# Optimization experiments

Hardware: AMD Instinct MI355X
Metric: run time of the kernel (lower is better)

Reference implementation:

```python
import jax, jax.numpy as jnp
import numpy as np

B, S, D_MODEL, D_HEAD = 8, 2048, 1024, 128
MAX_ROUNDS = 3
THRESH = 0.1
SCALE = 1.0 / np.sqrt(float(D_HEAD))


def setup_inputs() -> dict:
    key = jax.random.key(0)
    ks = jax.random.split(key, 12)

    def lin(k, out_d, in_d):
        # torch Linear weight layout [out, in], y = x @ W.T + b
        return (jax.random.normal(k, (out_d, in_d), jnp.float32) / np.sqrt(float(in_d))).astype(jnp.float32)

    thesis_w = lin(ks[3], D_HEAD, D_HEAD)
    return {
        "x": jax.random.normal(ks[0], (B, S, D_MODEL), jnp.float32),
        "wq": lin(ks[1], D_HEAD, D_MODEL),
        "wk": lin(ks[2], D_HEAD, D_MODEL),
        "wv": lin(ks[4], D_HEAD, D_MODEL),
        "thesis_w": thesis_w,  # antithesis weight is -thesis_w per __init__
        "thesis_b": 0.02 * jax.random.normal(ks[5], (D_HEAD,), jnp.float32),
        "anti_b": 0.02 * jax.random.normal(ks[6], (D_HEAD,), jnp.float32),
        "s_w1": lin(ks[7], D_HEAD, 3 * D_HEAD),
        "s_b1": jnp.zeros((D_HEAD,), jnp.float32),
        "s_w2": lin(ks[8], D_HEAD, D_HEAD),
        "s_b2": jnp.zeros((D_HEAD,), jnp.float32),
        "g_w": lin(ks[9], 1, 2 * D_HEAD),
        "g_b": jnp.zeros((1,), jnp.float32),
    }


def reference(x, wq, wk, wv, thesis_w, thesis_b, anti_b, s_w1, s_b1, s_w2, s_b2, g_w, g_b):
    # q/k/v projections (no bias)
    q = jnp.einsum("bsm,hm->bsh", x, wq)
    k = jnp.einsum("bsm,hm->bsh", x, wk)
    v = jnp.einsum("bsm,hm->bsh", x, wv)

    attn = jax.nn.softmax(jnp.einsum("bqh,bkh->bqk", q, k) * SCALE, axis=-1)
    # dropout is identity at eval time
    cur = jnp.einsum("bqk,bkh->bqh", attn, v)  # [B,S,Dh]

    # attn_weights and v never change across rounds, so thesis/antithesis are
    # round-invariant: compute the context projections once.
    context = cur
    thesis = context @ thesis_w.T + thesis_b
    anti = context @ (-thesis_w).T + anti_b  # antithesis weight = -thesis weight

    active = jnp.ones((B, S), dtype=bool)
    for _ in range(MAX_ROUNDS):
        # emulate `if not active_mask.any(): break` under jit
        any_active = jnp.any(active)
        am = active[..., None].astype(x.dtype)
        at, aa, ac = thesis * am, anti * am, cur * am

        h = jax.nn.relu(jnp.concatenate([at, aa, ac], axis=-1) @ s_w1.T + s_b1)
        synth = h @ s_w2.T + s_b2
        gate = jax.nn.sigmoid(jnp.concatenate([ac, synth], axis=-1) @ g_w.T + g_b)
        update = gate * (synth - ac) * 0.1
        new = cur + update  # applied to ALL tokens, matching original

        stable = jnp.linalg.norm(update, axis=-1) < THRESH  # new - cur == update
        cur = jnp.where(any_active, new, cur)
        active = jnp.where(any_active, active & ~stable, active)
    return cur
```

## Files before the change

### kernel.cpp

```cpp
#include <hip/hip_runtime.h>
#include <hip/hip_bf16.h>

#define B_   8
#define S_   2048
#define DM   1024
#define DH   128
#define BS_  16384
#define SCALE_  0.08838834764831845f
#define SCALE2_ 0.12751744f

typedef unsigned short u16;
typedef unsigned int   u32;
typedef _Float16 half8 __attribute__((ext_vector_type(8)));
typedef __bf16   bf16x8 __attribute__((ext_vector_type(8)));
typedef float    f32x4 __attribute__((ext_vector_type(4)));
typedef u32      u32x4 __attribute__((ext_vector_type(4)));

union H8 { u32x4 v; u32 u[4]; half8 h; bf16x8 b; };

__device__ __forceinline__ float bf2f(u16 u) {
    union { u32 i; float f; } w; w.i = ((u32)u) << 16; return w.f;
}
__device__ __forceinline__ void unpack8(uint4 v, float* f) {
    f[0] = bf2f(v.x & 0xffff); f[1] = bf2f(v.x >> 16);
    f[2] = bf2f(v.y & 0xffff); f[3] = bf2f(v.y >> 16);
    f[4] = bf2f(v.z & 0xffff); f[5] = bf2f(v.z >> 16);
    f[6] = bf2f(v.w & 0xffff); f[7] = bf2f(v.w >> 16);
}
__device__ __forceinline__ float ldE(const void* b, size_t i, int isbf16) {
    return isbf16 ? bf2f(((const u16*)b)[i]) : ((const float*)b)[i];
}
__device__ __forceinline__ void ld8(const void* b, size_t i, int isbf16, float* f) {
    if (isbf16) {
        unpack8(*(const uint4*)((const u16*)b + i), f);
    } else {
        float4 a = *(const float4*)((const float*)b + i);
        float4 c = *(const float4*)((const float*)b + i + 4);
        f[0] = a.x; f[1] = a.y; f[2] = a.z; f[3] = a.w;
        f[4] = c.x; f[5] = c.y; f[6] = c.z; f[7] = c.w;
    }
}
__device__ __forceinline__ u32 f2pk(float v) {
    _Float16 h = (_Float16)v;
    _Float16 l = (_Float16)(v - (float)h);
    union { _Float16 f; u16 u; } a, b; a.f = h; b.f = l;
    return ((u32)a.u << 16) | (u32)b.u;
}
__device__ __forceinline__ void split8(const float* f, u32x4& hi, u32x4& lo) {
    u32 H[8], L[8];
#pragma unroll
    for (int j = 0; j < 8; ++j) {
        _Float16 h = (_Float16)f[j];
        _Float16 l = (_Float16)(f[j] - (float)h);
        union { _Float16 x; u16 u; } a, b; a.x = h; b.x = l;
        H[j] = a.u; L[j] = b.u;
    }
    hi = (u32x4){H[0] | (H[1] << 16), H[2] | (H[3] << 16), H[4] | (H[5] << 16), H[6] | (H[7] << 16)};
    lo = (u32x4){L[0] | (L[1] << 16), L[2] | (L[3] << 16), L[4] | (L[5] << 16), L[6] | (L[7] << 16)};
}
__device__ __forceinline__ u32 permHI(u32 eB, u32 eA) { return __builtin_amdgcn_perm(eB, eA, 0x07060302u); }
__device__ __forceinline__ u16 f2h(float v) { union { _Float16 f; u16 u; } a; a.f = (_Float16)v; return a.u; }
__device__ __forceinline__ float h2f(u16 u) { union { _Float16 f; u16 u; } a; a.u = u; return (float)a.f; }

__global__ void init_kernel(const void* x, int* flag, int* active, int* counts) {
    int i = blockIdx.x * 256 + threadIdx.x;
    if (i < BS_) active[i] = 1;
    if (i < 4) counts[i] = (i == 0) ? BS_ : 0;
    if (i == 0) {
        const u16* w = (const u16*)x;
        int sane = 0;
        for (int t = 0; t < 256; ++t) {
            int e = (w[2 * t] >> 7) & 0xFF;
            if (e >= 100 && e <= 135) ++sane;
        }
        *flag = (sane >= 192) ? 1 : 0;
    }
}

__global__ __launch_bounds__(256) void prepack_w_kernel(
    const void* __restrict__ wq, const void* __restrict__ wk, const void* __restrict__ wv,
    const int* __restrict__ flag, u32x4* __restrict__ wpk)
{
    const int isb = *flag;
    const int gid = blockIdx.x * 256 + threadIdx.x;
    const int l  = gid & 63;
    const int t  = (gid >> 6) & 7;
    const int ks = (gid >> 9) & 31;
    const int z  = gid >> 14;
    const void* W = (z == 0) ? wq : (z == 1) ? wk : wv;
    const int row = 16 * t + (l & 15);
    const int k0  = ks * 32 + 8 * (l >> 4);
    const size_t base = ((((size_t)z * 32 + ks) * 16) + 2 * t) * 64 + l;
    if (isb) {
        uint4 v = *(const uint4*)((const u16*)W + (size_t)row * DM + k0);
        wpk[base] = (u32x4){v.x, v.y, v.z, v.w};
    } else {
        float f[8];
        ld8(W, (size_t)row * DM + k0, 0, f);
        u32x4 hi, lo;
        split8(f, hi, lo);
        wpk[base]      = hi;
        wpk[base + 64] = lo;
    }
}

__global__ __launch_bounds__(256) void qkv_kernel(
    const void* __restrict__ x, const u32x4* __restrict__ wpk,
    const int* __restrict__ flag, u32* __restrict__ qout,
    u32x4* __restrict__ kfrag, u32x4* __restrict__ vfrag)
{
    const int isb = *flag;
    const int z = blockIdx.z;
    const int bx = blockIdx.x;
    const int m0 = ((bx & 7) * 32 + (bx >> 3)) * 64;
    const int tid = threadIdx.x;
    const int wave = tid >> 6, lane = tid & 63;
    const int qd = lane >> 4, c = lane & 15;

    __shared__ u32x4 WLraw[2][16][64];
    u32x4 (*WLb)[2][8][64] = (u32x4(*)[2][8][64])WLraw;
    u32x4 (*WLf)[8][2][64] = (u32x4(*)[8][2][64])WLraw;
    u16 (*TS)[136] = (u16(*)[136])WLraw;

    const u32x4* wz = wpk + (size_t)z * (32 * 16 * 64);
    const size_t arow = (size_t)(m0 + wave * 16 + c) * DM + 8 * qd;

#define STAGE2(i_, b_)                                                            \
    {                                                                             \
        _Pragma("unroll")                                                         \
        for (int _j = 0; _j < 4; ++_j) {                                          \
            const int _g = wave * 4 + _j, _ksub = _g >> 3, _t = _g & 7;           \
            __builtin_amdgcn_global_load_lds(                                     \
                (const __attribute__((address_space(1))) u32*)(                   \
                    wz + ((size_t)(2 * (i_) + _ksub) * 16 + 2 * _t) * 64 + lane), \
                (__attribute__((address_space(3))) u32*)&WLb[b_][_ksub][_t][0],   \
                16, 0, 0);                                                        \
        }                                                                         \
    }
#define STAGE_W(ks_, b_)                                                          \
    {                                                                             \
        const u32x4* _src = wz + ((size_t)(ks_) * 16 + 4 * wave) * 64 + lane;     \
        _Pragma("unroll")                                                         \
        for (int _j = 0; _j < 4; ++_j) {                                          \
            __builtin_amdgcn_global_load_lds(                                     \
                (const __attribute__((address_space(1))) u32*)(_src + _j * 64),   \
                (__attribute__((address_space(3))) u32*)&WLf[b_][2 * wave + (_j >> 1)][_j & 1][0], \
                16, 0, 0);                                                        \
        }                                                                         \
    }

    f32x4 acc[8] = {};

    if (isb) {
        const u16* xb = (const u16*)x;
        uint4 A0 = *(const uint4*)(xb + arow);
        uint4 A1 = *(const uint4*)(xb + arow + 32);
        STAGE2(0, 0);
        uint4 A0n = *(const uint4*)(xb + arow + 64);
        uint4 A1n = *(const uint4*)(xb + arow + 96);
        __syncthreads();
        for (int i = 0; i < 16; ++i) {
            const int cb = i & 1;
            if (i + 1 < 16) STAGE2(i + 1, cb ^ 1);
            H8 Ah0; Ah0.v = (u32x4){A0.x, A0.y, A0.z, A0.w};
            H8 Ah1; Ah1.v = (u32x4){A1.x, A1.y, A1.z, A1.w};
#pragma unroll
            for (int t = 0; t < 8; ++t) {
                H8 bh; bh.v = WLb[cb][0][t][lane];
                acc[t] = __builtin_amdgcn_mfma_f32_16x16x32_bf16(Ah0.b, bh.b, acc[t], 0, 0, 0);
            }
#pragma unroll
            for (int t = 0; t < 8; ++t) {
                H8 bh; bh.v = WLb[cb][1][t][lane];
                acc[t] = __builtin_amdgcn_mfma_f32_16x16x32_bf16(Ah1.b, bh.b, acc[t], 0, 0, 0);
            }
            A0 = A0n; A1 = A1n;
            if (i + 2 < 16) {
                A0n = *(const uint4*)(xb + arow + (size_t)(i + 2) * 64);
                A1n = *(const uint4*)(xb + arow + (size_t)(i + 2) * 64 + 32);
            }
            __syncthreads();
        }
    } else {
        float Ar[8], Arn[8];
        ld8(x, arow, 0, Ar);
        STAGE_W(0, 0);
        ld8(x, arow + 32, 0, Arn);
        __syncthreads();
        for (int ks = 0; ks < 32; ++ks) {
            const int cb = ks & 1;
            if (ks + 1 < 32) STAGE_W(ks + 1, cb ^ 1);
            H8 Ah, Al;
            split8(Ar, Ah.v, Al.v);
#pragma unroll
            for (int t = 0; t < 8; ++t) {
                H8 bh, bl;
                bh.v = WLf[cb][t][0][lane]; bl.v = WLf[cb][t][1][lane];
                acc[t] = __builtin_amdgcn_mfma_f32_16x16x32_f16(Al.h, bh.h, acc[t], 0, 0, 0);
                acc[t] = __builtin_amdgcn_mfma_f32_16x16x32_f16(Ah.h, bl.h, acc[t], 0, 0, 0);
                acc[t] = __builtin_amdgcn_mfma_f32_16x16x32_f16(Ah.h, bh.h, acc[t], 0, 0, 0);
            }
#pragma unroll
            for (int j = 0; j < 8; ++j) Ar[j] = Arn[j];
            if (ks + 2 < 32) ld8(x, arow + (size_t)(ks + 2) * 32, 0, Arn);
            __syncthreads();
        }
    }
#undef STAGE2
#undef STAGE_W

    if (z == 0) {
#pragma unroll
        for (int r = 0; r < 4; ++r) {
            const int row = m0 + wave * 16 + qd * 4 + r;
            u32* op = qout + (size_t)row * DH + c;
#pragma unroll
            for (int t = 0; t < 8; ++t) op[t * 16] = f2pk(acc[t][r]);
        }
    } else {
#pragma unroll
        for (int t = 0; t < 8; ++t)
#pragma unroll
            for (int r = 0; r < 4; ++r)
                TS[wave * 16 + qd * 4 + r][16 * t + c] = f2h(acc[t][r]);
        __syncthreads();
        if (z == 1) {
#pragma unroll
            for (int i = 0; i < 4; ++i) {
                const int f = tid + 256 * i;
                const int lf = f & 63, ks = (f >> 6) & 3, sub = f >> 8;
                const int key = sub * 16 + (lf & 15);
                const int d0  = ks * 32 + 8 * (lf >> 4);
                u32 w[4];
#pragma unroll
                for (int q = 0; q < 4; ++q)
                    w[q] = (u32)TS[key][d0 + 2 * q] | ((u32)TS[key][d0 + 2 * q + 1] << 16);
                kfrag[((size_t)(m0 / 16 + sub) * 4 + ks) * 64 + lf] = (u32x4){w[0], w[1], w[2], w[3]};
            }
        } else {
#pragma unroll
            for (int i = 0; i < 4; ++i) {
                const int f = tid + 256 * i;
                const int lf = f & 63, t = (f >> 6) & 7, sub = f >> 9;
                const int kb2 = sub * 32 + 8 * (lf >> 4);
                const int dh  = 16 * t + (lf & 15);
                u32 w[4];
#pragma unroll
                for (int q = 0; q < 4; ++q)
                    w[q] = (u32)TS[kb2 + 2 * q][dh] | ((u32)TS[kb2 + 2 * q + 1][dh] << 16);
                vfrag[((size_t)(m0 / 32 + sub) * 8 + t) * 64 + lf] = (u32x4){w[0], w[1], w[2], w[3]};
            }
        }
    }
}

template <bool WRITE_PARTIAL>
__device__ __forceinline__ void attn_body(
    const u32* qp, const u32x4* __restrict__ kfrag, const u32x4* __restrict__ vfrag,
    u16* outO, u16* outL, float* cur,
    int b, int q0, int kt0, int kt1, int part)
{
    const int tid = threadIdx.x;
    const int wave = tid >> 6, lane = tid & 63;
    const int qd = lane >> 4, c = lane & 15;

    __shared__ __align__(16) u16 PB[4][640];

    H8 Qh[4];
    {
        const u32* qr = qp + ((size_t)b * S_ + q0 + wave * 16 + c) * DH;
#pragma unroll
        for (int ks = 0; ks < 4; ++ks) {
            uint4 e0 = *(const uint4*)(qr + ks * 32 + qd * 8);
            uint4 e1 = *(const uint4*)(qr + ks * 32 + qd * 8 + 4);
            Qh[ks].u[0] = permHI(e0.y, e0.x); Qh[ks].u[1] = permHI(e0.w, e0.z);
            Qh[ks].u[2] = permHI(e1.y, e1.x); Qh[ks].u[3] = permHI(e1.w, e1.z);
        }
    }

    f32x4 O[8] = {};
    float lsum[4] = {};

    const u32x4* kb0 = kfrag + (size_t)b * 128 * 256;
    const u32x4* vb0 = vfrag + (size_t)b * 64 * 512;

    for (int kt = kt0; kt < kt1; ++kt) {
        const u32x4* kf = kb0 + (size_t)kt * 512;
        const u32x4* vf = vb0 + (size_t)kt * 512;

        f32x4 S0 = {}, S1 = {};
        __builtin_amdgcn_s_setprio(1);
#pragma unroll
        for (int ks = 0; ks < 4; ++ks) {
            H8 kh;
            kh.v = kf[ks * 64 + lane];
            S0 = __builtin_amdgcn_mfma_f32_16x16x32_f16(Qh[ks].h, kh.h, S0, 0, 0, 0);
            kh.v = kf[256 + ks * 64 + lane];
            S1 = __builtin_amdgcn_mfma_f32_16x16x32_f16(Qh[ks].h, kh.h, S1, 0, 0, 0);
        }
        __builtin_amdgcn_s_setprio(0);

        u16* pw = PB[wave];
#pragma unroll
        for (int r = 0; r < 4; ++r) {
            float e0 = exp2f(fmaf(S0[r], SCALE2_, -4.0f));
            float e1 = exp2f(fmaf(S1[r], SCALE2_, -4.0f));
            lsum[r] += e0 + e1;
            pw[(4 * qd + r) * 40 + c]      = f2h(e0);
            pw[(4 * qd + r) * 40 + 16 + c] = f2h(e1);
        }

        uint4 ev = *(const uint4*)&pw[c * 40 + 8 * qd];
        H8 Ph;
        Ph.u[0] = ev.x; Ph.u[1] = ev.y; Ph.u[2] = ev.z; Ph.u[3] = ev.w;

        __builtin_amdgcn_s_setprio(1);
#pragma unroll
        for (int t = 0; t < 8; ++t) {
            H8 vh;
            vh.v = vf[t * 64 + lane];
            O[t] = __builtin_amdgcn_mfma_f32_16x16x32_f16(Ph.h, vh.h, O[t], 0, 0, 0);
        }
        __builtin_amdgcn_s_setprio(0);
    }

    if (WRITE_PARTIAL) {
        float lred[4];
#pragma unroll
        for (int r = 0; r < 4; ++r) {
            float l = lsum[r];
            l += __shfl_xor(l, 1); l += __shfl_xor(l, 2);
            l += __shfl_xor(l, 4); l += __shfl_xor(l, 8);
            lred[r] = l;
        }
        const size_t rb = (size_t)b * S_ + q0 + wave * 16 + 4 * qd;
        u16* Op = outO + (size_t)part * ((size_t)BS_ * DH);
#pragma unroll
        for (int t = 0; t < 8; ++t)
#pragma unroll
            for (int r = 0; r < 4; ++r)
                Op[(rb + r) * DH + t * 16 + c] = f2h(O[t][r]);
        if (c == 0) {
            u16* lp = outL + (size_t)part * BS_;
#pragma unroll
            for (int r = 0; r < 4; ++r) lp[rb + r] = f2h(lred[r]);
        }
    } else {
        float linv[4];
#pragma unroll
        for (int r = 0; r < 4; ++r) {
            float l = lsum[r];
            l += __shfl_xor(l, 1); l += __shfl_xor(l, 2);
            l += __shfl_xor(l, 4); l += __shfl_xor(l, 8);
            linv[r] = 1.0f / l;
        }
        const size_t rb = (size_t)b * S_ + q0 + wave * 16 + 4 * qd;
#pragma unroll
        for (int t = 0; t < 8; ++t)
#pragma unroll
            for (int r = 0; r < 4; ++r)
                cur[(rb + r) * DH + t * 16 + c] = O[t][r] * linv[r];
    }
}

__global__ __launch_bounds__(256) void attn_kernel(
    const u32* qp, const u32x4* __restrict__ kfrag, const u32x4* __restrict__ vfrag, float* cur)
{
    const int rid = blockIdx.x + 32 * blockIdx.y;
    attn_body<false>(qp, kfrag, vfrag, nullptr, nullptr, cur,
                     rid & 7, ((rid >> 3) & 31) * 64, 0, S_ / 32, 0);
}

__global__ __launch_bounds__(256) void attn_split_kernel(
    const u32* qp, const u32x4* __restrict__ kfrag, const u32x4* __restrict__ vfrag,
    u16* __restrict__ Opart, u16* __restrict__ lpart)
{
    const int rid = blockIdx.x + 32 * (blockIdx.y + 8 * blockIdx.z);
    const int b    = rid & 7;
    const int qx   = (rid >> 3) & 31;
    const int part = rid >> 8;
    const int quart = S_ / 128;
    attn_body<true>(qp, kfrag, vfrag, Opart, lpart, nullptr,
                    b, qx * 64, part * quart, (part + 1) * quart, part);
}

__global__ __launch_bounds__(256) void prepack_rw_kernel(
    const void* __restrict__ tw, const void* __restrict__ w1, const void* __restrict__ w2,
    const int* __restrict__ flag, u32x4* __restrict__ pk)
{
    const int isb = *flag;
    const int gid = blockIdx.x * 256 + threadIdx.x;
    const int l = gid & 63, t = (gid >> 6) & 7, ks = (gid >> 9) & 3, mat = gid >> 11;
    const int row = 16 * t + (l & 15);
    const int k0  = ks * 32 + 8 * (l >> 4);
    float f[8];
    if (mat == 0)      ld8(tw, (size_t)row * DH + k0, isb, f);
    else if (mat <= 3) ld8(w1, (size_t)row * 384 + (mat - 1) * 128 + k0, isb, f);
    else               ld8(w2, (size_t)row * DH + k0, isb, f);
    u32x4 hi, lo;
    split8(f, hi, lo);
    const size_t base = (((size_t)mat * 4 + ks) * 16 + 2 * t) * 64 + l;
    pk[base] = hi; pk[base + 64] = lo;
}

struct Afrag { H8 h[4], l[4]; };
__device__ __forceinline__ void splitA(const float (&A)[4][8], Afrag& F) {
#pragma unroll
    for (int ks = 0; ks < 4; ++ks) split8(A[ks], F.h[ks].v, F.l[ks].v);
}

__global__ __launch_bounds__(256) void round0_kernel(
    const float* __restrict__ cur0g,
    const u16* __restrict__ Opart, const u16* __restrict__ lpart,
    const u32x4* __restrict__ pk, u16* __restrict__ T0,
    const void* __restrict__ tb, const void* __restrict__ ab,
    const void* __restrict__ b1, const void* __restrict__ b2,
    const void* __restrict__ gw, const void* __restrict__ gb,
    const int* __restrict__ flag, int* active, int* counts,
    float* cur_out, int combine)
{
    const int isb = *flag;
    const int tok0 = blockIdx.x * 16;
    const int tid = threadIdx.x;
    const int wave = tid >> 6, lane = tid & 63;
    const int qd = lane >> 4, c = lane & 15;

    __shared__ u32x4 WB[2][2][8][64];
    __shared__ u16 TS[16][132];
    __shared__ float CS[16][128];
    __shared__ float tbS[128], abS[128], b1S[128], b2S[128], gwS[256];
    __shared__ int blkcnt;

    auto stageBh = [&](int mat, int h) {
#pragma unroll
        for (int j = 0; j < 4; ++j) {
            const int g = wave * 4 + j, kl = g >> 3, t = g & 7;
            __builtin_amdgcn_global_load_lds(
                (const __attribute__((address_space(1))) u32*)(
                    pk + (((size_t)mat * 4 + 2 * h + kl) * 16 + 2 * t) * 64 + lane),
                (__attribute__((address_space(3))) u32*)&WB[h][kl][t][0],
                16, 0, 0);
        }
    };
    auto gemmBh = [&](const Afrag& F, int h, f32x4 (&acc)[2]) {
#pragma unroll
        for (int kl = 0; kl < 2; ++kl) {
            const int ks = 2 * h + kl;
#pragma unroll
            for (int tl = 0; tl < 2; ++tl) {
                H8 bh; bh.v = WB[h][kl][2 * wave + tl][lane];
                acc[tl] = __builtin_amdgcn_mfma_f32_16x16x32_f16(F.l[ks].h, bh.h, acc[tl], 0, 0, 0);
                acc[tl] = __builtin_amdgcn_mfma_f32_16x16x32_f16(F.h[ks].h, bh.h, acc[tl], 0, 0, 0);
            }
        }
    };
    auto stageFq = [&](int mat, int q, int buf) {
#pragma unroll
        for (int j = 0; j < 4; ++j) {
            const int g = wave * 4 + j, p = g & 1, t = g >> 1;
            __builtin_amdgcn_global_load_lds(
                (const __attribute__((address_space(1))) u32*)(
                    pk + (((size_t)mat * 4 + q) * 16 + 2 * t + p) * 64 + lane),
                (__attribute__((address_space(3))) u32*)&WB[buf][p][t][0],
                16, 0, 0);
        }
    };
    auto gemmFq = [&](const Afrag& F, int q, int buf, f32x4 (&acc)[2]) {
#pragma unroll
        for (int tl = 0; tl < 2; ++tl) {
            H8 bh, bl;
            bh.v = WB[buf][0][2 * wave + tl][lane];
            bl.v = WB[buf][1][2 * wave + tl][lane];
            acc[tl] = __builtin_amdgcn_mfma_f32_16x16x32_f16(F.l[q].h, bh.h, acc[tl], 0, 0, 0);
            acc[tl] = __builtin_amdgcn_mfma_f32_16x16x32_f16(F.h[q].h, bl.h, acc[tl], 0, 0, 0);
            acc[tl] = __builtin_amdgcn_mfma_f32_16x16x32_f16(F.h[q].h, bh.h, acc[tl], 0, 0, 0);
        }
    };
    auto GEMMF = [&](int mat, const Afrag& F, f32x4 (&acc)[2]) {
        for (int q = 0; q < 4; ++q) {
            stageFq(mat, q, q & 1);
            __syncthreads();
            gemmFq(F, q, q & 1, acc);
            __syncthreads();
        }
    };

    const int hr = 4 * qd;
    const int rowl = c;

    auto writeTS = [&](const f32x4 (&acc)[2], const float* bias, bool relu) {
#pragma unroll
        for (int tl = 0; tl < 2; ++tl)
#pragma unroll
            for (int rr = 0; rr < 4; ++rr) {
                const int col = 16 * (2 * wave + tl) + c;
                float v = acc[tl][rr] + (bias ? bias[col] : 0.0f);
                TS[hr + rr][col] = f2h(relu ? fmaxf(v, 0.0f) : v);
            }
    };
    auto buildA1 = [&](Afrag& F) {
        float Ac[4][8];
#pragma unroll
        for (int ks = 0; ks < 4; ++ks)
#pragma unroll
            for (int j = 0; j < 8; ++j)
                Ac[ks][j] = CS[rowl][ks * 32 + 8 * qd + j];
        splitA(Ac, F);
    };
    auto buildAt = [&](Afrag& F) {
        float Ac[4][8];
#pragma unroll
        for (int ks = 0; ks < 4; ++ks)
#pragma unroll
            for (int j = 0; j < 8; ++j) {
                const int k = ks * 32 + 8 * qd + j;
                Ac[ks][j] = h2f(TS[rowl][k]) + tbS[k];
            }
        splitA(Ac, F);
    };
    auto buildAa = [&](Afrag& F) {
        float Ac[4][8];
#pragma unroll
        for (int ks = 0; ks < 4; ++ks)
#pragma unroll
            for (int j = 0; j < 8; ++j) {
                const int k = ks * 32 + 8 * qd + j;
                Ac[ks][j] = abS[k] - h2f(TS[rowl][k]);
            }
        splitA(Ac, F);
    };
    auto buildAh = [&](Afrag& F) {
        float Ac[4][8];
#pragma unroll
        for (int ks = 0; ks < 4; ++ks)
#pragma unroll
            for (int j = 0; j < 8; ++j)
                Ac[ks][j] = h2f(TS[rowl][ks * 32 + 8 * qd + j]);
        splitA(Ac, F);
    };

    if (tid < 128) {
        tbS[tid] = ldE(tb, tid, isb); abS[tid] = ldE(ab, tid, isb);
        b1S[tid] = ldE(b1, tid, isb); b2S[tid] = ldE(b2, tid, isb);
    }
    gwS[tid] = ldE(gw, tid, isb);
    if (tid == 0) blkcnt = 0;
    const float gbf = ldE(gb, 0, isb);
    {
        const int row = tid >> 4, d0 = (tid & 15) * 8;
        float a8[8];
        if (combine) {
            const size_t grow = (size_t)(tok0 + row);
            const float lt = h2f(lpart[grow]) + h2f(lpart[BS_ + grow])
                           + h2f(lpart[2 * BS_ + grow]) + h2f(lpart[3 * BS_ + grow]);
            const float linv = 1.0f / lt;
            float acc[8] = {};
            const size_t N1 = (size_t)BS_ * DH;
#pragma unroll
            for (int p = 0; p < 4; ++p) {
                const u16* op = Opart + (size_t)p * N1 + grow * DH + d0;
                uint4 v0 = *(const uint4*)op;
                const u32 w[4] = {v0.x, v0.y, v0.z, v0.w};
#pragma unroll
                for (int j = 0; j < 4; ++j) {
                    acc[2 * j]     += h2f((u16)(w[j] & 0xffff));
                    acc[2 * j + 1] += h2f((u16)(w[j] >> 16));
                }
            }
#pragma unroll
            for (int e = 0; e < 8; ++e) a8[e] = acc[e] * linv;
        } else {
            const float* cr = cur0g + (size_t)(tok0 + row) * DH + d0;
            float4 v0 = *(const float4*)cr;
            float4 v1 = *(const float4*)(cr + 4);
            a8[0] = v0.x; a8[1] = v0.y; a8[2] = v0.z; a8[3] = v0.w;
            a8[4] = v1.x; a8[5] = v1.y; a8[6] = v1.z; a8[7] = v1.w;
        }
#pragma unroll
        for (int e = 0; e < 8; ++e) CS[row][d0 + e] = a8[e];
    }

    if (isb) {
        stageBh(0, 0);
        __syncthreads();
        Afrag FA; buildA1(FA);
        stageBh(0, 1);
        f32x4 accT[2] = {};
        gemmBh(FA, 0, accT);
        __syncthreads();
        stageBh(1, 0);
        gemmBh(FA, 1, accT);
        writeTS(accT, nullptr, false);
        __syncthreads();
        for (int i = tid; i < 16 * 64; i += 256) {
            const int row = i >> 6, c2 = (i & 63) * 2;
            *(u32*)&T0[(size_t)(tok0 + row) * DH + c2] = *(const u32*)&TS[row][c2];
        }
        f32x4 acc1[2] = {};
        {
            Afrag FC; buildAt(FC);
            stageBh(1, 1);
            gemmBh(FC, 0, acc1);
            __syncthreads();
            stageBh(2, 0);
            gemmBh(FC, 1, acc1);
            __syncthreads();
        }
        {
            Afrag FC; buildAa(FC);
            stageBh(2, 1);
            gemmBh(FC, 0, acc1);
            __syncthreads();
            stageBh(3, 0);
            gemmBh(FC, 1, acc1);
            __syncthreads();
        }
        {
            Afrag FC; buildA1(FC);
            stageBh(3, 1);
            gemmBh(FC, 0, acc1);
            __syncthreads();
            stageBh(4, 0);
            gemmBh(FC, 1, acc1);
        }
        writeTS(acc1, b1S, true);
        __syncthreads();
        {
            Afrag FC; buildAh(FC);
            stageBh(4, 1);
            f32x4 acc2[2] = {};
            gemmBh(FC, 0, acc2);
            __syncthreads();
            gemmBh(FC, 1, acc2);
            writeTS(acc2, b2S, false);
        }
        __syncthreads();
    } else {
        __syncthreads();
        Afrag FA; buildA1(FA);
        f32x4 accT[2] = {};
        GEMMF(0, FA, accT);
        writeTS(accT, nullptr, false);
        __syncthreads();
        for (int i = tid; i < 16 * 64; i += 256) {
            const int row = i >> 6, c2 = (i & 63) * 2;
            *(u32*)&T0[(size_t)(tok0 + row) * DH + c2] = *(const u32*)&TS[row][c2];
        }
        f32x4 acc1[2] = {};
        { Afrag FC; buildAt(FC); GEMMF(1, FC, acc1); }
        { Afrag FC; buildAa(FC); GEMMF(2, FC, acc1); }
        { Afrag FC; buildA1(FC); GEMMF(3, FC, acc1); }
        writeTS(acc1, b1S, true);
        __syncthreads();
        {
            Afrag FC; buildAh(FC);
            f32x4 acc2[2] = {};
            GEMMF(4, FC, acc2);
            writeTS(acc2, b2S, false);
        }
        __syncthreads();
    }

    const int tok = tid >> 4, d0g = (tid & 15) * 8;
    float cv[8];
#pragma unroll
    for (int e = 0; e < 8; ++e) cv[e] = CS[tok][d0g + e];
    float srow[8];
#pragma unroll
    for (int e = 0; e < 8; ++e) srow[e] = h2f(TS[tok][d0g + e]);
    float gp = 0.0f;
#pragma unroll
    for (int e = 0; e < 8; ++e)
        gp += cv[e] * gwS[d0g + e] + srow[e] * gwS[128 + d0g + e];
    gp += __shfl_xor(gp, 1, 16);
    gp += __shfl_xor(gp, 2, 16);
    gp += __shfl_xor(gp, 4, 16);
    gp += __shfl_xor(gp, 8, 16);
    const float gate = 1.0f / (1.0f + __expf(-(gp + gbf)));
    float ss = 0.0f; float up[8];
#pragma unroll
    for (int e = 0; e < 8; ++e) {
        float u = gate * (srow[e] - cv[e]) * 0.1f;
        up[e] = u; ss += u * u;
    }
    ss += __shfl_xor(ss, 1, 16);
    ss += __shfl_xor(ss, 2, 16);
    ss += __shfl_xor(ss, 4, 16);
    ss += __shfl_xor(ss, 8, 16);
    const bool stable = sqrtf(ss) < 0.1f;

    float* op = cur_out + (size_t)(tok0 + tok) * DH + d0g;
    *(float4*)op       = make_float4(cv[0] + up[0], cv[1] + up[1], cv[2] + up[2], cv[3] + up[3]);
    *(float4*)(op + 4) = make_float4(cv[4] + up[4], cv[5] + up[5], cv[6] + up[6], cv[7] + up[7]);
    const int newact = stable ? 0 : 1;
    if ((tid & 15) == 0) {
        active[tok0 + tok] = newact;
        if (newact) atomicAdd(&blkcnt, 1);
    }
    __syncthreads();
    if (tid == 0 && blkcnt > 0) atomicAdd(&counts[1], blkcnt);
}

__global__ __launch_bounds__(256) void round_kernel(
    const float* curr,
    const u32x4* __restrict__ pk, const u16* __restrict__ T0,
    const void* __restrict__ tb, const void* __restrict__ ab,
    const void* __restrict__ b1, const void* __restrict__ b2,
    const void* __restrict__ gw, const void* __restrict__ gb,
    const int* __restrict__ flag, int* active, int* counts, int r,
    float* cur_out, void* dout)
{
    const int isb = *flag;
    const int tok0 = blockIdx.x * 32;
    const int tid = threadIdx.x;
    const bool last = (dout != nullptr);

    if (counts[r] <= 0) {
        if (last) {
            for (int e = tid; e < 32 * DH; e += 256) {
                size_t idx = (size_t)tok0 * DH + e;
                float v = curr[idx];
                if (isb) ((__hip_bfloat16*)dout)[idx] = __float2bfloat16(v);
                else     ((float*)dout)[idx] = v;
            }
        }
        return;
    }

    const int wave = tid >> 6, lane = tid & 63;
    const int qd = lane >> 4, c = lane & 15;
    const int rowg = wave >> 1, colh = wave & 1;

    __shared__ u32x4 WB[2][4][8][64];
    __shared__ u16 TS[32][132];
    __shared__ float actS[32], tbS[128], abS[128], b1S[128], b2S[128], gwS[256];
    __shared__ int blkcnt;

    auto stageB = [&](int mat, int buf) {
#pragma unroll
        for (int j = 0; j < 8; ++j) {
            const int g = wave * 8 + j, ks = g >> 3, t = g & 7;
            __builtin_amdgcn_global_load_lds(
                (const __attribute__((address_space(1))) u32*)(
                    pk + (((size_t)mat * 4 + ks) * 16 + 2 * t) * 64 + lane),
                (__attribute__((address_space(3))) u32*)&WB[buf][ks][t][0],
                16, 0, 0);
        }
    };
    auto stageF = [&](int mat, int h, int buf) {
#pragma unroll
        for (int j = 0; j < 8; ++j) {
            const int g = wave * 8 + j, kl = g >> 4, p = (g >> 3) & 1, t = g & 7;
            __builtin_amdgcn_global_load_lds(
                (const __attribute__((address_space(1))) u32*)(
                    pk + (((size_t)mat * 4 + 2 * h + kl) * 16 + 2 * t + p) * 64 + lane),
                (__attribute__((address_space(3))) u32*)&WB[buf][kl * 2 + p][t][0],
                16, 0, 0);
        }
    };
    auto gemmB = [&](const Afrag& F, int buf, f32x4 (&acc)[4]) {
#pragma unroll
        for (int ks = 0; ks < 4; ++ks)
#pragma unroll
            for (int tl = 0; tl < 4; ++tl) {
                H8 bh; bh.v = WB[buf][ks][4 * colh + tl][lane];
                acc[tl] = __builtin_amdgcn_mfma_f32_16x16x32_f16(F.l[ks].h, bh.h, acc[tl], 0, 0, 0);
                acc[tl] = __builtin_amdgcn_mfma_f32_16x16x32_f16(F.h[ks].h, bh.h, acc[tl], 0, 0, 0);
            }
    };
    auto gemmFh = [&](const Afrag& F, int h, int buf, f32x4 (&acc)[4]) {
#pragma unroll
        for (int kl = 0; kl < 2; ++kl) {
            const int ks = 2 * h + kl;
#pragma unroll
            for (int tl = 0; tl < 4; ++tl) {
                H8 bh, bl;
                bh.v = WB[buf][kl * 2][4 * colh + tl][lane];
                bl.v = WB[buf][kl * 2 + 1][4 * colh + tl][lane];
                acc[tl] = __builtin_amdgcn_mfma_f32_16x16x32_f16(F.l[ks].h, bh.h, acc[tl], 0, 0, 0);
                acc[tl] = __builtin_amdgcn_mfma_f32_16x16x32_f16(F.h[ks].h, bl.h, acc[tl], 0, 0, 0);
                acc[tl] = __builtin_amdgcn_mfma_f32_16x16x32_f16(F.h[ks].h, bh.h, acc[tl], 0, 0, 0);
            }
        }
    };
    auto STAGE = [&](int mat, int buf) { if (isb) stageB(mat, buf); else stageF(mat, 0, buf); };
    auto GEMM = [&](int mat, const Afrag& F, int buf, f32x4 (&acc)[4]) {
        if (isb) {
            gemmB(F, buf, acc);
        } else {
            gemmFh(F, 0, buf, acc);
            __syncthreads();
            stageF(mat, 1, buf);
            __syncthreads();
            gemmFh(F, 1, buf, acc);
        }
    };

    STAGE(1, 1);
    if (tid < 32) actS[tid] = active[tok0 + tid] ? 1.0f : 0.0f;
    if (tid < 128) {
        tbS[tid] = ldE(tb, tid, isb); abS[tid] = ldE(ab, tid, isb);
        b1S[tid] = ldE(b1, tid, isb); b2S[tid] = ldE(b2, tid, isb);
    }
    gwS[tid] = ldE(gw, tid, isb);
    if (tid == 0) blkcnt = 0;
    const float gbf = ldE(gb, 0, isb);

    const int rowl = 16 * rowg + c;
    const int hr   = 16 * rowg + 4 * qd;

    for (int i = tid; i < 32 * 64; i += 256) {
        const int row = i >> 6, c2 = (i & 63) * 2;
        *(u32*)&TS[row][c2] = *(const u32*)&T0[(size_t)(tok0 + row) * DH + c2];
    }
    __syncthreads();

    STAGE(2, 0);
    f32x4 acc1[4] = {};
    const float am_r = actS[rowl];
    {
        float Ac[4][8];
#pragma unroll
        for (int ks = 0; ks < 4; ++ks)
#pragma unroll
            for (int j = 0; j < 8; ++j) {
                const int k = ks * 32 + 8 * qd + j;
                Ac[ks][j] = (h2f(TS[rowl][k]) + tbS[k]) * am_r;
            }
        Afrag FC; splitA(Ac, FC);
        GEMM(1, FC, 1, acc1);
    }
    __syncthreads();

    STAGE(3, 1);
    {
        float Ac[4][8];
#pragma unroll
        for (int ks = 0; ks < 4; ++ks)
#pragma unroll
            for (int j = 0; j < 8; ++j) {
                const int k = ks * 32 + 8 * qd + j;
                Ac[ks][j] = (abS[k] - h2f(TS[rowl][k])) * am_r;
            }
        Afrag FC; splitA(Ac, FC);
        GEMM(2, FC, 0, acc1);
    }
    __syncthreads();

    STAGE(4, 0);
    {
        float Ac[4][8];
        const float* cr = curr + (size_t)(tok0 + rowl) * DH;
#pragma unroll
        for (int ks = 0; ks < 4; ++ks) {
            float4 a0 = *(const float4*)(cr + ks * 32 + 8 * qd);
            float4 a1 = *(const float4*)(cr + ks * 32 + 8 * qd + 4);
            Ac[ks][0] = a0.x * am_r; Ac[ks][1] = a0.y * am_r;
            Ac[ks][2] = a0.z * am_r; Ac[ks][3] = a0.w * am_r;
            Ac[ks][4] = a1.x * am_r; Ac[ks][5] = a1.y * am_r;
            Ac[ks][6] = a1.z * am_r; Ac[ks][7] = a1.w * am_r;
        }
        Afrag FC; splitA(Ac, FC);
        GEMM(3, FC, 1, acc1);
    }
#pragma unroll
    for (int tl = 0; tl < 4; ++tl)
#pragma unroll
        for (int rr = 0; rr < 4; ++rr) {
            const int col = 16 * (4 * colh + tl) + c;
            TS[hr + rr][col] = f2h(fmaxf(acc1[tl][rr] + b1S[col], 0.0f));
        }
    __syncthreads();

    {
        float Ac[4][8];
#pragma unroll
        for (int ks = 0; ks < 4; ++ks)
#pragma unroll
            for (int j = 0; j < 8; ++j)
                Ac[ks][j] = h2f(TS[rowl][ks * 32 + 8 * qd + j]);
        Afrag FC; splitA(Ac, FC);
        f32x4 acc2[4] = {};
        GEMM(4, FC, 0, acc2);
        __syncthreads();
#pragma unroll
        for (int tl = 0; tl < 4; ++tl)
#pragma unroll
            for (int rr = 0; rr < 4; ++rr) {
                const int col = 16 * (4 * colh + tl) + c;
                TS[hr + rr][col] = f2h(acc2[tl][rr] + b2S[col]);
            }
    }
    __syncthreads();

    const int tok = tid >> 3, d0 = (tid & 7) * 16;
    const float am = actS[tok];
    const float* cp = curr + (size_t)(tok0 + tok) * DH + d0;
    float cv[16];
#pragma unroll
    for (int t = 0; t < 4; ++t) {
        float4 vv = *(const float4*)(cp + t * 4);
        cv[t * 4] = vv.x; cv[t * 4 + 1] = vv.y; cv[t * 4 + 2] = vv.z; cv[t * 4 + 3] = vv.w;
    }
    float srow[16];
#pragma unroll
    for (int e = 0; e < 16; ++e) srow[e] = h2f(TS[tok][d0 + e]);
    float gp = 0.0f;
#pragma unroll
    for (int e = 0; e < 16; ++e)
        gp += cv[e] * am * gwS[d0 + e] + srow[e] * gwS[128 + d0 + e];
    gp += __shfl_xor(gp, 1, 8);
    gp += __shfl_xor(gp, 2, 8);
    gp += __shfl_xor(gp, 4, 8);
    const float gate = 1.0f / (1.0f + __expf(-(gp + gbf)));
    float ss = 0.0f; float up[16];
#pragma unroll
    for (int e = 0; e < 16; ++e) {
        float u = gate * (srow[e] - cv[e] * am) * 0.1f;
        up[e] = u; ss += u * u;
    }
    ss += __shfl_xor(ss, 1, 8);
    ss += __shfl_xor(ss, 2, 8);
    ss += __shfl_xor(ss, 4, 8);
    const bool stable = sqrtf(ss) < 0.1f;

    if (last) {
        size_t off = (size_t)(tok0 + tok) * DH + d0;
        if (isb) {
            __hip_bfloat16* op = (__hip_bfloat16*)dout + off;
#pragma unroll
            for (int e = 0; e < 16; ++e) op[e] = __float2bfloat16(cv[e] + up[e]);
        } else {
            float* op = (float*)dout + off;
#pragma unroll
            for (int t = 0; t < 4; ++t)
                *(float4*)(op + t * 4) = make_float4(cv[t * 4] + up[t * 4], cv[t * 4 + 1] + up[t * 4 + 1],
                                                     cv[t * 4 + 2] + up[t * 4 + 2], cv[t * 4 + 3] + up[t * 4 + 3]);
        }
    } else {
        float* op = cur_out + (size_t)(tok0 + tok) * DH + d0;
#pragma unroll
        for (int t = 0; t < 4; ++t)
            *(float4*)(op + t * 4) = make_float4(cv[t * 4] + up[t * 4], cv[t * 4 + 1] + up[t * 4 + 1],
                                                 cv[t * 4 + 2] + up[t * 4 + 2], cv[t * 4 + 3] + up[t * 4 + 3]);
    }
    const int newact = (am > 0.0f && !stable) ? 1 : 0;
    if ((tid & 7) == 0) {
        active[tok0 + tok] = newact;
        if (newact) atomicAdd(&blkcnt, 1);
    }
    __syncthreads();
    if (tid == 0 && blkcnt > 0) atomicAdd(&counts[r + 1], blkcnt);
}

extern "C" void kernel_launch(void* const* d_in, const int* in_sizes, int n_in,
                              void* d_out, int out_size, void* d_ws, size_t ws_size,
                              hipStream_t stream) {
    const void* x  = d_in[0];
    const void* wq = d_in[1];
    const void* wk = d_in[2];
    const void* wv = d_in[3];
    const void* tw = d_in[4];
    const void* tb = d_in[5];
    const void* ab = d_in[6];
    const void* w1 = d_in[7];
    const void* b1 = d_in[8];
    const void* w2 = d_in[9];
    const void* b2 = d_in[10];
    const void* gw = d_in[11];
    const void* gb = d_in[12];

    u32* ws = (u32*)d_ws;
    const size_t N1 = (size_t)BS_ * DH;
    u32* qp = ws;
    u32* kp = ws + N1;
    u32* vp = ws + 2 * N1;
    int* active = (int*)(ws + 3 * N1);
    int* counts = active + BS_;
    int* flag   = counts + 4;
    float* cur0  = (float*)qp;
    float* cur_r = (float*)kp;
    u16* Opart16 = (u16*)(ws + 3 * N1 + 32768);
    u16* lpart16 = (u16*)(ws + 5 * N1 + 32768);
    const bool big_ws = ws_size >= (size_t)42300000;
    u32x4* wpk = (u32x4*)(ws + 3 * N1 + 32768);
    u32x4* pkRW = (u32x4*)vp;
    u16*   T0c  = (u16*)(vp + 131072);
    u32x4* kfragP = (u32x4*)kp;
    u32x4* vfragP = (u32x4*)vp;

    init_kernel<<<dim3(BS_ / 256), 256, 0, stream>>>(x, flag, active, counts);
    prepack_w_kernel<<<dim3(192), 256, 0, stream>>>(wq, wk, wv, flag, wpk);
    qkv_kernel<<<dim3(BS_ / 64, 1, 3), 256, 0, stream>>>(x, wpk, flag, qp, kfragP, vfragP);
    if (big_ws) {
        attn_split_kernel<<<dim3(S_ / 64, B_, 4), 256, 0, stream>>>(qp, kfragP, vfragP, Opart16, lpart16);
    } else {
        attn_kernel<<<dim3(S_ / 64, B_), 256, 0, stream>>>(qp, kfragP, vfragP, cur0);
    }
    prepack_rw_kernel<<<dim3(40), 256, 0, stream>>>(tw, w1, w2, flag, pkRW);
    round0_kernel<<<dim3(BS_ / 16), 256, 0, stream>>>(
        cur0, Opart16, lpart16, pkRW, T0c, tb, ab, b1, b2, gw, gb,
        flag, active, counts, cur_r, big_ws ? 1 : 0);
    round_kernel<<<dim3(BS_ / 32), 256, 0, stream>>>(
        cur_r, pkRW, T0c, tb, ab, b1, b2, gw, gb, flag, active, counts, 1, cur_r, nullptr);
    round_kernel<<<dim3(BS_ / 32), 256, 0, stream>>>(
        cur_r, pkRW, T0c, tb, ab, b1, b2, gw, gb, flag, active, counts, 2, cur_r, d_out);
}
```

Measured before the change: 253.2 us.

## Split QKV projection tile across 8 waves, halving per-wave output columns

The QKV projection kernel now launches 512 threads per block instead of 256. Pairs of waves share a 16-row group, and each wave computes half of the 128 output columns, holding 4 accumulators instead of 8. Weight staging into LDS and the fragment writeback loops are redistributed over the larger thread count. The aim is more waves in flight to hide latency and fewer accumulator registers per wave. The cost is that each A row fragment is now loaded from global memory by two waves, and 512-thread blocks may limit how many blocks fit per CU.

```diff
diff --git a/kernel.cpp b/kernel.cpp
--- a/kernel.cpp
+++ b/kernel.cpp
@@ -104,7 +104,7 @@
     }
 }
 
-__global__ __launch_bounds__(256) void qkv_kernel(
+__global__ __launch_bounds__(512) void qkv_kernel(
     const void* __restrict__ x, const u32x4* __restrict__ wpk,
     const int* __restrict__ flag, u32* __restrict__ qout,
     u32x4* __restrict__ kfrag, u32x4* __restrict__ vfrag)
@@ -116,6 +116,7 @@
     const int tid = threadIdx.x;
     const int wave = tid >> 6, lane = tid & 63;
     const int qd = lane >> 4, c = lane & 15;
+    const int rowg = wave >> 1, colh = wave & 1;
 
     __shared__ u32x4 WLraw[2][16][64];
     u32x4 (*WLb)[2][8][64] = (u32x4(*)[2][8][64])WLraw;
@@ -123,13 +124,13 @@
     u16 (*TS)[136] = (u16(*)[136])WLraw;
 
     const u32x4* wz = wpk + (size_t)z * (32 * 16 * 64);
-    const size_t arow = (size_t)(m0 + wave * 16 + c) * DM + 8 * qd;
+    const size_t arow = (size_t)(m0 + 16 * rowg + c) * DM + 8 * qd;
 
 #define STAGE2(i_, b_)                                                            \
     {                                                                             \
         _Pragma("unroll")                                                         \
-        for (int _j = 0; _j < 4; ++_j) {                                          \
-            const int _g = wave * 4 + _j, _ksub = _g >> 3, _t = _g & 7;           \
+        for (int _j = 0; _j < 2; ++_j) {                                          \
+            const int _g = wave * 2 + _j, _ksub = _g >> 3, _t = _g & 7;           \
             __builtin_amdgcn_global_load_lds(                                     \
                 (const __attribute__((address_space(1))) u32*)(                   \
                     wz + ((size_t)(2 * (i_) + _ksub) * 16 + 2 * _t) * 64 + lane), \
@@ -139,17 +140,18 @@
     }
 #define STAGE_W(ks_, b_)                                                          \
     {                                                                             \
-        const u32x4* _src = wz + ((size_t)(ks_) * 16 + 4 * wave) * 64 + lane;     \
         _Pragma("unroll")                                                         \
-        for (int _j = 0; _j < 4; ++_j) {                                          \
+        for (int _j = 0; _j < 2; ++_j) {                                          \
+            const int _s = wave * 2 + _j;                                         \
             __builtin_amdgcn_global_load_lds(                                     \
-                (const __attribute__((address_space(1))) u32*)(_src + _j * 64),   \
-                (__attribute__((address_space(3))) u32*)&WLf[b_][2 * wave + (_j >> 1)][_j & 1][0], \
+                (const __attribute__((address_space(1))) u32*)(                   \
+                    wz + ((size_t)(ks_) * 16 + _s) * 64 + lane),                  \
+                (__attribute__((address_space(3))) u32*)&WLf[b_][_s >> 1][_s & 1][0], \
                 16, 0, 0);                                                        \
         }                                                                         \
     }
 
-    f32x4 acc[8] = {};
+    f32x4 acc[4] = {};
 
     if (isb) {
         const u16* xb = (const u16*)x;
@@ -165,14 +167,14 @@
             H8 Ah0; Ah0.v = (u32x4){A0.x, A0.y, A0.z, A0.w};
             H8 Ah1; Ah1.v = (u32x4){A1.x, A1.y, A1.z, A1.w};
 #pragma unroll
-            for (int t = 0; t < 8; ++t) {
-                H8 bh; bh.v = WLb[cb][0][t][lane];
-                acc[t] = __builtin_amdgcn_mfma_f32_16x16x32_bf16(Ah0.b, bh.b, acc[t], 0, 0, 0);
-            }
-#pragma unroll
-            for (int t = 0; t < 8; ++t) {
-                H8 bh; bh.v = WLb[cb][1][t][lane];
-                acc[t] = __builtin_amdgcn_mfma_f32_16x16x32_bf16(Ah1.b, bh.b, acc[t], 0, 0, 0);
+            for (int tl = 0; tl < 4; ++tl) {
+                H8 bh; bh.v = WLb[cb][0][4 * colh + tl][lane];
+                acc[tl] = __builtin_amdgcn_mfma_f32_16x16x32_bf16(Ah0.b, bh.b, acc[tl], 0, 0, 0);
+            }
+#pragma unroll
+            for (int tl = 0; tl < 4; ++tl) {
+                H8 bh; bh.v = WLb[cb][1][4 * colh + tl][lane];
+                acc[tl] = __builtin_amdgcn_mfma_f32_16x16x32_bf16(Ah1.b, bh.b, acc[tl], 0, 0, 0);
             }
             A0 = A0n; A1 = A1n;
             if (i + 2 < 16) {
@@ -193,12 +195,13 @@
             H8 Ah, Al;
             split8(Ar, Ah.v, Al.v);
 #pragma unroll
-            for (int t = 0; t < 8; ++t) {
+            for (int tl = 0; tl < 4; ++tl) {
                 H8 bh, bl;
-                bh.v = WLf[cb][t][0][lane]; bl.v = WLf[cb][t][1][lane];
-                acc[t] = __builtin_amdgcn_mfma_f32_16x16x32_f16(Al.h, bh.h, acc[t], 0, 0, 0);
-                acc[t] = __builtin_amdgcn_mfma_f32_16x16x32_f16(Ah.h, bl.h, acc[t], 0, 0, 0);
-                acc[t] = __builtin_amdgcn_mfma_f32_16x16x32_f16(Ah.h, bh.h, acc[t], 0, 0, 0);
+                bh.v = WLf[cb][4 * colh + tl][0][lane];
+                bl.v = WLf[cb][4 * colh + tl][1][lane];
+                acc[tl] = __builtin_amdgcn_mfma_f32_16x16x32_f16(Al.h, bh.h, acc[tl], 0, 0, 0);
+                acc[tl] = __builtin_amdgcn_mfma_f32_16x16x32_f16(Ah.h, bl.h, acc[tl], 0, 0, 0);
+                acc[tl] = __builtin_amdgcn_mfma_f32_16x16x32_f16(Ah.h, bh.h, acc[tl], 0, 0, 0);
             }
 #pragma unroll
             for (int j = 0; j < 8; ++j) Ar[j] = Arn[j];
@@ -212,22 +215,22 @@
     if (z == 0) {
 #pragma unroll
         for (int r = 0; r < 4; ++r) {
-            const int row = m0 + wave * 16 + qd * 4 + r;
-            u32* op = qout + (size_t)row * DH + c;
-#pragma unroll
-            for (int t = 0; t < 8; ++t) op[t * 16] = f2pk(acc[t][r]);
+            const int row = m0 + 16 * rowg + 4 * qd + r;
+            u32* op = qout + (size_t)row * DH + 64 * colh + c;
+#pragma unroll
+            for (int tl = 0; tl < 4; ++tl) op[tl * 16] = f2pk(acc[tl][r]);
         }
     } else {
 #pragma unroll
-        for (int t = 0; t < 8; ++t)
+        for (int tl = 0; tl < 4; ++tl)
 #pragma unroll
             for (int r = 0; r < 4; ++r)
-                TS[wave * 16 + qd * 4 + r][16 * t + c] = f2h(acc[t][r]);
+                TS[16 * rowg + 4 * qd + r][16 * (4 * colh + tl) + c] = f2h(acc[tl][r]);
         __syncthreads();
         if (z == 1) {
 #pragma unroll
-            for (int i = 0; i < 4; ++i) {
-                const int f = tid + 256 * i;
+            for (int i = 0; i < 2; ++i) {
+                const int f = tid + 512 * i;
                 const int lf = f & 63, ks = (f >> 6) & 3, sub = f >> 8;
                 const int key = sub * 16 + (lf & 15);
                 const int d0  = ks * 32 + 8 * (lf >> 4);
@@ -239,8 +242,8 @@
             }
         } else {
 #pragma unroll
-            for (int i = 0; i < 4; ++i) {
-                const int f = tid + 256 * i;
+            for (int i = 0; i < 2; ++i) {
+                const int f = tid + 512 * i;
                 const int lf = f & 63, t = (f >> 6) & 7, sub = f >> 9;
                 const int kb2 = sub * 32 + 8 * (lf >> 4);
                 const int dh  = 16 * t + (lf & 15);
@@ -991,7 +994,7 @@
 
     init_kernel<<<dim3(BS_ / 256), 256, 0, stream>>>(x, flag, active, counts);
     prepack_w_kernel<<<dim3(192), 256, 0, stream>>>(wq, wk, wv, flag, wpk);
-    qkv_kernel<<<dim3(BS_ / 64, 1, 3), 256, 0, stream>>>(x, wpk, flag, qp, kfragP, vfragP);
+    qkv_kernel<<<dim3(BS_ / 64, 1, 3), 512, 0, stream>>>(x, wpk, flag, qp, kfragP, vfragP);
     if (big_ws) {
         attn_split_kernel<<<dim3(S_ / 64, B_, 4), 256, 0, stream>>>(qp, kfragP, vfragP, Opart16, lpart16);
     } else {
```

After: 287.3 us. 1.13x slower.
